# Kernel optimization log

Hardware: AMD Instinct MI355X
Metric: run time of the kernel (lower is better)

Reference implementation:

```python
import jax, jax.numpy as jnp
import numpy as np
from jax import lax

M, T, D, E, NTAGS = 512, 512, 128, 512, 74
GH = D // 2   # GRU hidden per direction (64)
LH = E // 2   # LSTM hidden per direction (256)


def _gru_dir(x, Wih, Whh, bih, bhh):
    # x: [T, Din] -> [T, H]; PyTorch gate order r, z, n
    h = Whh.shape[1]
    gi = x @ Wih.T + bih  # [T, 3H] precomputed input projections
    def step(hprev, gi_t):
        gh = hprev @ Whh.T + bhh
        r = jax.nn.sigmoid(gi_t[:h] + gh[:h])
        z = jax.nn.sigmoid(gi_t[h:2 * h] + gh[h:2 * h])
        n = jnp.tanh(gi_t[2 * h:] + r * gh[2 * h:])
        hnew = (1.0 - z) * n + z * hprev
        return hnew, hnew
    _, hs = lax.scan(step, jnp.zeros((h,), x.dtype), gi)
    return hs


def _bigru(x, Wf, Uf, bf, cf, Wb, Ub, bb, cb):
    hf = _gru_dir(x, Wf, Uf, bf, cf)
    hb = _gru_dir(x[::-1], Wb, Ub, bb, cb)[::-1]
    return jnp.concatenate([hf, hb], axis=-1)


def _lstm_dir(x, Wih, Whh, bih, bhh):
    # PyTorch gate order i, f, g, o
    h = Whh.shape[1]
    gi = x @ Wih.T + bih  # [T, 4H]
    def step(carry, gi_t):
        hprev, cprev = carry
        g = gi_t + hprev @ Whh.T + bhh
        i = jax.nn.sigmoid(g[:h])
        f = jax.nn.sigmoid(g[h:2 * h])
        gg = jnp.tanh(g[2 * h:3 * h])
        o = jax.nn.sigmoid(g[3 * h:])
        c = f * cprev + i * gg
        hnew = o * jnp.tanh(c)
        return (hnew, c), hnew
    init = (jnp.zeros((h,), x.dtype), jnp.zeros((h,), x.dtype))
    _, hs = lax.scan(step, init, gi)
    return hs


def _bilstm(x, Wf, Uf, bf, cf, Wb, Ub, bb, cb):
    hf = _lstm_dir(x, Wf, Uf, bf, cf)
    hb = _lstm_dir(x[::-1], Wb, Ub, bb, cb)[::-1]
    return jnp.concatenate([hf, hb], axis=-1)


def setup_inputs() -> dict:
    key = jax.random.key(0)
    ks = jax.random.split(key, 32)
    s = 0.05
    def n(k, shape, scale=s):
        return jax.random.normal(k, shape, jnp.float32) * scale
    inp = {
        'memory': jax.random.normal(ks[0], (M, T, D), jnp.float32),
        'u': jax.random.normal(ks[1], (T, D), jnp.float32),
        'embed': jax.random.normal(ks[2], (T, E), jnp.float32),
        'W_ff': n(ks[3], (D, 2 * D)), 'b_ff': n(ks[4], (D,)),
        'gWih_f': n(ks[5], (3 * GH, D)), 'gWhh_f': n(ks[6], (3 * GH, GH)),
        'gbih_f': n(ks[7], (3 * GH,)), 'gbhh_f': n(ks[8], (3 * GH,)),
        'gWih_b': n(ks[9], (3 * GH, D)), 'gWhh_b': n(ks[10], (3 * GH, GH)),
        'gbih_b': n(ks[11], (3 * GH,)), 'gbhh_b': n(ks[12], (3 * GH,)),
        'W_k': n(ks[13], (E, D)), 'b_k': n(ks[14], (E,)),
        'lWih_f': n(ks[15], (4 * LH, E)), 'lWhh_f': n(ks[16], (4 * LH, LH)),
        'lbih_f': n(ks[17], (4 * LH,)), 'lbhh_f': n(ks[18], (4 * LH,)),
        'lWih_b': n(ks[19], (4 * LH, E)), 'lWhh_b': n(ks[20], (4 * LH, LH)),
        'lbih_b': n(ks[21], (4 * LH,)), 'lbhh_b': n(ks[22], (4 * LH,)),
        'W_out': n(ks[23], (NTAGS, E)), 'b_out': n(ks[24], (NTAGS,)),
    }
    return inp


def reference(memory, u, embed, W_ff, b_ff,
              gWih_f, gWhh_f, gbih_f, gbhh_f,
              gWih_b, gWhh_b, gbih_b, gbhh_b,
              W_k, b_k,
              lWih_f, lWhh_f, lbih_f, lbhh_f,
              lWih_b, lWhh_b, lbih_b, lbhh_b,
              W_out, b_out):
    # --- memory attention (original: python loop over self._memory) ---
    # p[i] = <flatten(memory[i]), flatten(u)>; softmax over memories
    p = jax.nn.softmax(jnp.einsum('mtd,td->m', memory, u))  # [M]
    cat = jnp.concatenate([memory, jnp.broadcast_to(u, memory.shape)], axis=-1)  # [M,T,2D]
    g = cat @ W_ff.T + b_ff  # [M,T,D] (ff_layer applied per memory)
    G = jnp.einsum('m,mtd->td', p, g)  # weighted sum over memories [T,D]
    # --- session encoder (bidirectional GRU) ---
    h = _bigru(G, gWih_f, gWhh_f, gbih_f, gbhh_f, gWib := gWih_b, gWhh_b, gbih_b, gbhh_b)  # [T,D]
    # --- knowledge encoder ---
    o = (u + h) @ W_k.T + b_k  # [T,E]
    # --- tagging head: BiLSTM over embed + o, then linear + softmax ---
    x = embed + o
    comb = _bilstm(x, lWih_f, lWhh_f, lbih_f, lbhh_f, lWih_b, lWhh_b, lbih_b, lbhh_b)  # [T,E]
    logits = comb @ W_out.T + b_out  # [T, NTAGS]
    return jax.nn.softmax(logits, axis=-1)
```

## Files before the change

### kernel.cpp

```cpp
#include <hip/hip_runtime.h>
#include <math.h>

#define TT 512
#define DD 128
#define MM 512
#define EE 512
#define NTAGS 74
#define GH 64
#define LH 256

typedef _Float16 half_t;
typedef _Float16 v2h __attribute__((ext_vector_type(2)));
typedef _Float16 v8h __attribute__((ext_vector_type(8)));
typedef _Float16 v16h __attribute__((ext_vector_type(16)));
typedef int v4i __attribute__((ext_vector_type(4)));

__device__ __forceinline__ float fdot2f(v2h a, v2h b, float c) {
#if __has_builtin(__builtin_amdgcn_fdot2)
    return __builtin_amdgcn_fdot2(a, b, c, false);
#else
    return c + (float)a[0] * (float)b[0] + (float)a[1] * (float)b[1];
#endif
}

__device__ __forceinline__ int sdot4(int a, int b, int c) {
#if __has_builtin(__builtin_amdgcn_sdot4)
    return __builtin_amdgcn_sdot4(a, b, c, false);
#else
    return c + ((a << 24) >> 24) * ((b << 24) >> 24)
             + ((a << 16) >> 24) * ((b << 16) >> 24)
             + ((a << 8) >> 24) * ((b << 8) >> 24)
             + (a >> 24) * (b >> 24);
#endif
}

__device__ __forceinline__ float sigf(float x) { return 1.f / (1.f + __expf(-x)); }
__device__ __forceinline__ float tanhfast(float x) { return 1.f - 2.f / (__expf(2.f * x) + 1.f); }

__device__ __forceinline__ void lds_barrier() {
    __builtin_amdgcn_sched_barrier(0);
    asm volatile("s_waitcnt lgkmcnt(0)" ::: "memory");
    __builtin_amdgcn_s_barrier();
    __builtin_amdgcn_sched_barrier(0);
}

__device__ __forceinline__ void wave_lds_fence() {
    __builtin_amdgcn_sched_barrier(0);
    asm volatile("s_waitcnt lgkmcnt(0)" ::: "memory");
    __builtin_amdgcn_sched_barrier(0);
}

__device__ __forceinline__ v16h load16(const float* p) {
    float4 x0 = ((const float4*)p)[0];
    float4 x1 = ((const float4*)p)[1];
    float4 x2 = ((const float4*)p)[2];
    float4 x3 = ((const float4*)p)[3];
    v16h r;
    r[0] = (half_t)x0.x; r[1] = (half_t)x0.y; r[2] = (half_t)x0.z; r[3] = (half_t)x0.w;
    r[4] = (half_t)x1.x; r[5] = (half_t)x1.y; r[6] = (half_t)x1.z; r[7] = (half_t)x1.w;
    r[8] = (half_t)x2.x; r[9] = (half_t)x2.y; r[10] = (half_t)x2.z; r[11] = (half_t)x2.w;
    r[12] = (half_t)x3.x; r[13] = (half_t)x3.y; r[14] = (half_t)x3.z; r[15] = (half_t)x3.w;
    return r;
}

#define OPAQUE4(a, b, c, d) \
    asm volatile("" : "+v"(a), "+v"(b), "+v"(c), "+v"(d))

__device__ __forceinline__ void dot16(const v16h& w, const v8h& h0, const v8h& h1,
                                      float& x0, float& x1) {
    x0 = fdot2f(v2h{w[0], w[1]}, v2h{h0[0], h0[1]}, x0);
    x1 = fdot2f(v2h{w[2], w[3]}, v2h{h0[2], h0[3]}, x1);
    x0 = fdot2f(v2h{w[4], w[5]}, v2h{h0[4], h0[5]}, x0);
    x1 = fdot2f(v2h{w[6], w[7]}, v2h{h0[6], h0[7]}, x1);
    x0 = fdot2f(v2h{w[8], w[9]}, v2h{h1[0], h1[1]}, x0);
    x1 = fdot2f(v2h{w[10], w[11]}, v2h{h1[2], h1[3]}, x1);
    x0 = fdot2f(v2h{w[12], w[13]}, v2h{h1[4], h1[5]}, x0);
    x1 = fdot2f(v2h{w[14], w[15]}, v2h{h1[6], h1[7]}, x1);
}

__device__ __forceinline__ int pack4(int b0, int b1, int b2, int b3) {
    return (b0 & 0xff) | ((b1 & 0xff) << 8) | ((b2 & 0xff) << 16) | (b3 << 24);
}

__device__ __forceinline__ v4i quant16(const float* p, float inv_s) {
    float4 x0 = ((const float4*)p)[0];
    float4 x1 = ((const float4*)p)[1];
    float4 x2 = ((const float4*)p)[2];
    float4 x3 = ((const float4*)p)[3];
    v4i r;
    r.x = pack4(__float2int_rn(x0.x * inv_s), __float2int_rn(x0.y * inv_s),
                __float2int_rn(x0.z * inv_s), __float2int_rn(x0.w * inv_s));
    r.y = pack4(__float2int_rn(x1.x * inv_s), __float2int_rn(x1.y * inv_s),
                __float2int_rn(x1.z * inv_s), __float2int_rn(x1.w * inv_s));
    r.z = pack4(__float2int_rn(x2.x * inv_s), __float2int_rn(x2.y * inv_s),
                __float2int_rn(x2.z * inv_s), __float2int_rn(x2.w * inv_s));
    r.w = pack4(__float2int_rn(x3.x * inv_s), __float2int_rn(x3.y * inv_s),
                __float2int_rn(x3.z * inv_s), __float2int_rn(x3.w * inv_s));
    return r;
}

__device__ __forceinline__ float rowmax128(const float* p) {
    float m = 0.f;
#pragma unroll 8
    for (int k = 0; k < 128; k += 4) {
        float4 a = *(const float4*)(p + k);
        m = fmaxf(m, fmaxf(fmaxf(fabsf(a.x), fabsf(a.y)), fmaxf(fabsf(a.z), fabsf(a.w))));
    }
    return m;
}

__global__ __launch_bounds__(256) void k_dots(const float* __restrict__ mem,
                                              const float* __restrict__ u,
                                              float* __restrict__ dots) {
    int m = blockIdx.x;
    const float4* m4 = (const float4*)(mem + (size_t)m * TT * DD);
    const float4* u4 = (const float4*)u;
    float acc = 0.f;
#pragma unroll 4
    for (int it = 0; it < (TT * DD / 4) / 256; ++it) {
        int i = it * 256 + threadIdx.x;
        float4 a = m4[i], b = u4[i];
        acc += a.x * b.x + a.y * b.y + a.z * b.z + a.w * b.w;
    }
    for (int off = 32; off; off >>= 1) acc += __shfl_down(acc, off, 64);
    __shared__ float red[4];
    int w = threadIdx.x >> 6, l = threadIdx.x & 63;
    if (l == 0) red[w] = acc;
    __syncthreads();
    if (threadIdx.x == 0) dots[m] = red[0] + red[1] + red[2] + red[3];
}

__global__ __launch_bounds__(512) void k_softmax_p(const float* __restrict__ dots,
                                                   float* __restrict__ p) {
    int tid = threadIdx.x;
    float v = dots[tid];
    float mx = v;
    for (int off = 32; off; off >>= 1) mx = fmaxf(mx, __shfl_down(mx, off, 64));
    __shared__ float red[8];
    __shared__ float bm, bs;
    int w = tid >> 6, l = tid & 63;
    if (l == 0) red[w] = mx;
    __syncthreads();
    if (tid == 0) {
        float t = red[0];
        for (int i = 1; i < 8; ++i) t = fmaxf(t, red[i]);
        bm = t;
    }
    __syncthreads();
    float e = __expf(v - bm);
    float sm = e;
    for (int off = 32; off; off >>= 1) sm += __shfl_down(sm, off, 64);
    if (l == 0) red[w] = sm;
    __syncthreads();
    if (tid == 0) {
        float t = 0.f;
        for (int i = 0; i < 8; ++i) t += red[i];
        bs = t;
    }
    __syncthreads();
    p[tid] = e / bs;
}

__global__ __launch_bounds__(128) void k_wsum(const float* __restrict__ mem,
                                              const float* __restrict__ p,
                                              float* __restrict__ Mbar) {
    __shared__ float pl[MM];
    for (int i = threadIdx.x; i < MM; i += 128) pl[i] = p[i];
    __syncthreads();
    int i4 = blockIdx.x * 128 + threadIdx.x;
    const float4* m4 = (const float4*)mem;
    float4 acc = {0.f, 0.f, 0.f, 0.f};
#pragma unroll 4
    for (int m = 0; m < MM; ++m) {
        float pm = pl[m];
        float4 a = m4[(size_t)m * (TT * DD / 4) + i4];
        acc.x += pm * a.x; acc.y += pm * a.y; acc.z += pm * a.z; acc.w += pm * a.w;
    }
    ((float4*)Mbar)[i4] = acc;
}

__global__ __launch_bounds__(128) void k_G(const float* __restrict__ Mbar,
                                           const float* __restrict__ u,
                                           const float* __restrict__ Wff,
                                           const float* __restrict__ bff,
                                           float* __restrict__ G) {
    int t = blockIdx.x, d = threadIdx.x;
    __shared__ __align__(16) float Ml[DD], ul[DD];
    Ml[d] = Mbar[t * DD + d];
    ul[d] = u[t * DD + d];
    __syncthreads();
    const float* wr = Wff + (size_t)d * 2 * DD;
    float a0 = 0.f, a1 = 0.f;
#pragma unroll 4
    for (int k = 0; k < DD; ++k) {
        a0 += Ml[k] * wr[k];
        a1 += ul[k] * wr[DD + k];
    }
    G[t * DD + d] = a0 + a1 + bff[d];
}

__global__ __launch_bounds__(384) void k_gru_gi(const float* __restrict__ G,
                                                const float* __restrict__ Wf,
                                                const float* __restrict__ bf,
                                                const float* __restrict__ Wb,
                                                const float* __restrict__ bb,
                                                float* __restrict__ gi) {
    int t = blockIdx.x;
    __shared__ __align__(16) float Gl[DD];
    if (threadIdx.x < DD) Gl[threadIdx.x] = G[t * DD + threadIdx.x];
    __syncthreads();
    int r = threadIdx.x;
    const float* w;
    float b;
    float* o;
    if (r < 192) {
        w = Wf + (size_t)r * DD; b = bf[r]; o = gi + ((size_t)0 * TT + t) * 192 + r;
    } else {
        int rr = r - 192;
        w = Wb + (size_t)rr * DD; b = bb[rr]; o = gi + ((size_t)1 * TT + t) * 192 + rr;
    }
    float a0 = 0.f, a1 = 0.f;
#pragma unroll 4
    for (int k = 0; k < DD; k += 2) {
        a0 += Gl[k] * w[k];
        a1 += Gl[k + 1] * w[k + 1];
    }
    *o = a0 + a1 + b;
}

__global__ __launch_bounds__(64) void k_gru_seq(const float* __restrict__ Whh_f,
                                                const float* __restrict__ bhh_f,
                                                const float* __restrict__ Whh_b,
                                                const float* __restrict__ bhh_b,
                                                const float* __restrict__ gi,
                                                float* __restrict__ hbuf) {
    int dir = blockIdx.x;
    int u = threadIdx.x;
    const float* Whh = dir ? Whh_b : Whh_f;
    const float* bhh = dir ? bhh_b : bhh_f;
    const float* wr_ = Whh + (size_t)u * 64;
    const float* wz_ = Whh + (size_t)(64 + u) * 64;
    const float* wn_ = Whh + (size_t)(128 + u) * 64;
    v16h wr0 = load16(wr_), wr1 = load16(wr_ + 16), wr2 = load16(wr_ + 32), wr3 = load16(wr_ + 48);
    v16h wz0 = load16(wz_), wz1 = load16(wz_ + 16), wz2 = load16(wz_ + 32), wz3 = load16(wz_ + 48);
    v16h wn0 = load16(wn_), wn1 = load16(wn_ + 16), wn2 = load16(wn_ + 32), wn3 = load16(wn_ + 48);
    OPAQUE4(wr0, wr1, wr2, wr3);
    OPAQUE4(wz0, wz1, wz2, wz3);
    OPAQUE4(wn0, wn1, wn2, wn3);
    float bh_r = bhh[u], bh_z = bhh[64 + u], bh_n = bhh[128 + u];

    __shared__ __align__(16) half_t hl[64];
    hl[u] = (half_t)0.f;
    float h = 0.f;
    int t0 = dir ? (TT - 1) : 0;
    const float* g0p = gi + ((size_t)dir * TT + t0) * 192;
    float g_r = g0p[u], g_z = g0p[64 + u], g_n = g0p[128 + u];
    wave_lds_fence();

    for (int s = 0; s < TT; ++s) {
        int t = dir ? (TT - 1 - s) : s;
        int sn = (s + 1 < TT) ? (s + 1) : s;
        int tn = dir ? (TT - 1 - sn) : sn;
        const float* gb = gi + ((size_t)dir * TT + tn) * 192;
        float pn_r = gb[u], pn_z = gb[64 + u], pn_n = gb[128 + u];

        const v8h* hv = (const v8h*)hl;
        v8h h0 = hv[0], h1 = hv[1], h2 = hv[2], h3 = hv[3];
        v8h h4 = hv[4], h5 = hv[5], h6 = hv[6], h7 = hv[7];
        float ar0 = bh_r, ar1 = 0.f, az0 = bh_z, az1 = 0.f, an0 = bh_n, an1 = 0.f;
        dot16(wr0, h0, h1, ar0, ar1); dot16(wr1, h2, h3, ar0, ar1);
        dot16(wr2, h4, h5, ar0, ar1); dot16(wr3, h6, h7, ar0, ar1);
        dot16(wz0, h0, h1, az0, az1); dot16(wz1, h2, h3, az0, az1);
        dot16(wz2, h4, h5, az0, az1); dot16(wz3, h6, h7, az0, az1);
        dot16(wn0, h0, h1, an0, an1); dot16(wn1, h2, h3, an0, an1);
        dot16(wn2, h4, h5, an0, an1); dot16(wn3, h6, h7, an0, an1);

        float r = sigf(g_r + ar0 + ar1);
        float z = sigf(g_z + az0 + az1);
        float n = tanhfast(g_n + r * (an0 + an1));
        h = (1.f - z) * n + z * h;
        hbuf[t * DD + dir * 64 + u] = h;
        hl[u] = (half_t)h;
        wave_lds_fence();
        g_r = pn_r; g_z = pn_z; g_n = pn_n;
    }
}

__global__ __launch_bounds__(512) void k_x(const float* __restrict__ u,
                                           const float* __restrict__ hbuf,
                                           const float* __restrict__ Wk,
                                           const float* __restrict__ bk,
                                           const float* __restrict__ embed,
                                           float* __restrict__ x) {
    int t = blockIdx.x, e = threadIdx.x;
    __shared__ __align__(16) float sl[DD];
    if (e < DD) sl[e] = u[t * DD + e] + hbuf[t * DD + e];
    __syncthreads();
    const float* wr = Wk + (size_t)e * DD;
    float a0 = 0.f, a1 = 0.f;
#pragma unroll 4
    for (int k = 0; k < DD; k += 2) {
        a0 += sl[k] * wr[k];
        a1 += sl[k + 1] * wr[k + 1];
    }
    x[t * EE + e] = embed[t * EE + e] + a0 + a1 + bk[e];
}

__global__ __launch_bounds__(1024) void k_lstm_gi(const float* __restrict__ x,
                                                  const float* __restrict__ Wf,
                                                  const float* __restrict__ bf,
                                                  const float* __restrict__ Wb,
                                                  const float* __restrict__ bb,
                                                  float* __restrict__ gi) {
    int dir = blockIdx.y;
    int t0 = blockIdx.x * 8;
    __shared__ __align__(16) float xl[8 * EE];
    for (int i = threadIdx.x; i < 8 * EE; i += 1024) xl[i] = x[(size_t)t0 * EE + i];
    __syncthreads();
    int r = threadIdx.x;
    const float* W = dir ? Wb : Wf;
    const float* bi = dir ? bb : bf;
    const float* wr = W + (size_t)r * EE;
    float b = bi[r];
    float acc[8];
#pragma unroll
    for (int uu = 0; uu < 8; ++uu) acc[uu] = b;
    for (int k = 0; k < EE; k += 4) {
        float4 wv = *(const float4*)(wr + k);
#pragma unroll
        for (int uu = 0; uu < 8; ++uu) {
            float4 xv = *(const float4*)(&xl[uu * EE + k]);
            acc[uu] += wv.x * xv.x + wv.y * xv.y + wv.z * xv.z + wv.w * xv.w;
        }
    }
#pragma unroll
    for (int uu = 0; uu < 8; ++uu)
        gi[((size_t)dir * TT + (t0 + uu)) * 1024 + r] = acc[uu];
}

__global__ __launch_bounds__(512, 2) void k_lstm_seq(const float* __restrict__ Whh_f,
                                                     const float* __restrict__ bhh_f,
                                                     const float* __restrict__ Whh_b,
                                                     const float* __restrict__ bhh_b,
                                                     const float* __restrict__ gi,
                                                     float* __restrict__ comb) {
    int dir = blockIdx.x;
    int tid = threadIdx.x;
    int u = tid >> 1;
    int half = tid & 1;
    const float* Whh = dir ? Whh_b : Whh_f;
    const float* bhh = dir ? bhh_b : bhh_f;

    __shared__ __align__(16) int hq[2][64];

    const float* ri = Whh + (size_t)u * 256 + half * 128;
    const float* rf = Whh + (size_t)(256 + u) * 256 + half * 128;
    const float* rg = Whh + (size_t)(512 + u) * 256 + half * 128;
    const float* ro = Whh + (size_t)(768 + u) * 256 + half * 128;

    float mi = rowmax128(ri); mi = fmaxf(mi, __shfl_xor(mi, 1, 64));
    float mf = rowmax128(rf); mf = fmaxf(mf, __shfl_xor(mf, 1, 64));
    float mg = rowmax128(rg); mg = fmaxf(mg, __shfl_xor(mg, 1, 64));
    float mo = rowmax128(ro); mo = fmaxf(mo, __shfl_xor(mo, 1, 64));
    float inv_i = 127.f / mi, inv_f = 127.f / mf, inv_g = 127.f / mg, inv_o = 127.f / mo;
    float fs_i = mi / 16129.f, fs_f = mf / 16129.f, fs_g = mg / 16129.f, fs_o = mo / 16129.f;

#define DECLROW(P, ptr, inv)                                                      \
    v4i P##0 = quant16((ptr), (inv)),       P##1 = quant16((ptr) + 16, (inv)),    \
        P##2 = quant16((ptr) + 32, (inv)),  P##3 = quant16((ptr) + 48, (inv)),    \
        P##4 = quant16((ptr) + 64, (inv)),  P##5 = quant16((ptr) + 80, (inv)),    \
        P##6 = quant16((ptr) + 96, (inv)),  P##7 = quant16((ptr) + 112, (inv));   \
    OPAQUE4(P##0, P##1, P##2, P##3);                                              \
    OPAQUE4(P##4, P##5, P##6, P##7)

    DECLROW(wi, ri, inv_i);
    DECLROW(wf, rf, inv_f);
    DECLROW(wg, rg, inv_g);
    DECLROW(wo, ro, inv_o);
#undef DECLROW

    float bh_i = bhh[u], bh_f = bhh[256 + u], bh_g = bhh[512 + u], bh_o = bhh[768 + u];
    if (tid < 64) hq[0][tid] = 0;
    float c_state = 0.f;
    int tfirst = dir ? (TT - 1) : 0;
    const float* gp0 = gi + ((size_t)dir * TT + tfirst) * 1024;
    float g_i = gp0[u], g_f = gp0[256 + u], g_g = gp0[512 + u], g_o = gp0[768 + u];
    lds_barrier();

#define ROWD1(P, c, A0, A1)                                          \
    A0 = sdot4(P##c.x, hv##c.x, A0); A1 = sdot4(P##c.y, hv##c.y, A1); \
    A0 = sdot4(P##c.z, hv##c.z, A0); A1 = sdot4(P##c.w, hv##c.w, A1)
#define ROWDOT(P, A0, A1)                                                  \
    ROWD1(P, 0, A0, A1); ROWD1(P, 1, A0, A1); ROWD1(P, 2, A0, A1);         \
    ROWD1(P, 3, A0, A1); ROWD1(P, 4, A0, A1); ROWD1(P, 5, A0, A1);         \
    ROWD1(P, 6, A0, A1); ROWD1(P, 7, A0, A1)

    for (int s = 0; s < TT; ++s) {
        int t = dir ? (TT - 1 - s) : s;
        int sn = (s + 1 < TT) ? (s + 1) : s;
        int tn = dir ? (TT - 1 - sn) : sn;
        const float* gb = gi + ((size_t)dir * TT + tn) * 1024;
        float pn_i = gb[u], pn_f = gb[256 + u], pn_g = gb[512 + u], pn_o = gb[768 + u];

        const v4i* hb = (const v4i*)&hq[s & 1][half * 32];
        v4i hv0 = hb[0], hv1 = hb[1], hv2 = hb[2], hv3 = hb[3];
        v4i hv4 = hb[4], hv5 = hb[5], hv6 = hb[6], hv7 = hb[7];
        int ai0 = 0, ai1 = 0, af0 = 0, af1 = 0, ag0 = 0, ag1 = 0, ao0 = 0, ao1 = 0;
        ROWDOT(wi, ai0, ai1);
        ROWDOT(wf, af0, af1);
        ROWDOT(wg, ag0, ag1);
        ROWDOT(wo, ao0, ao1);
        int ai = ai0 + ai1; ai += __shfl_xor(ai, 1, 64);
        int af = af0 + af1; af += __shfl_xor(af, 1, 64);
        int ag = ag0 + ag1; ag += __shfl_xor(ag, 1, 64);
        int ao = ao0 + ao1; ao += __shfl_xor(ao, 1, 64);

        float iv = sigf((float)ai * fs_i + bh_i + g_i);
        float fv = sigf((float)af * fs_f + bh_f + g_f);
        float gv = tanhfast((float)ag * fs_g + bh_g + g_g);
        float ov = sigf((float)ao * fs_o + bh_o + g_o);
        c_state = fv * c_state + iv * gv;
        float hval = ov * tanhfast(c_state);
        if (half == 0) {
            comb[(size_t)t * EE + dir * 256 + u] = hval;
            ((signed char*)hq[(s + 1) & 1])[u] = (signed char)__float2int_rn(hval * 127.f);
        }
        lds_barrier();
        g_i = pn_i; g_f = pn_f; g_g = pn_g; g_o = pn_o;
    }
#undef ROWDOT
#undef ROWD1
}

__global__ __launch_bounds__(128) void k_out(const float* __restrict__ comb,
                                             const float* __restrict__ Wout,
                                             const float* __restrict__ bout,
                                             float* __restrict__ out) {
    int t = blockIdx.x;
    __shared__ __align__(16) float cl[EE];
    __shared__ float ll[NTAGS];
    __shared__ float mred, sred;
    for (int i = threadIdx.x; i < EE; i += 128) cl[i] = comb[(size_t)t * EE + i];
    __syncthreads();
    int e = threadIdx.x;
    if (e < NTAGS) {
        const float* wr = Wout + (size_t)e * EE;
        float a0 = 0.f, a1 = 0.f;
#pragma unroll 4
        for (int k = 0; k < EE; k += 2) {
            a0 += cl[k] * wr[k];
            a1 += cl[k + 1] * wr[k + 1];
        }
        ll[e] = a0 + a1 + bout[e];
    }
    __syncthreads();
    if (threadIdx.x == 0) {
        float m = ll[0];
        for (int i = 1; i < NTAGS; ++i) m = fmaxf(m, ll[i]);
        float ss = 0.f;
        for (int i = 0; i < NTAGS; ++i) ss += __expf(ll[i] - m);
        mred = m;
        sred = ss;
    }
    __syncthreads();
    if (e < NTAGS) out[t * NTAGS + e] = __expf(ll[e] - mred) / sred;
}

#define OFF_DOTS  ((size_t)0)
#define OFF_P     ((size_t)512)
#define OFF_MBAR  ((size_t)1024)
#define OFF_G     ((size_t)66560)
#define OFF_GIG   ((size_t)132096)
#define OFF_HBUF  ((size_t)328704)
#define OFF_X     ((size_t)394240)
#define OFF_GIL   ((size_t)656384)
#define OFF_COMB  ((size_t)1704960)

extern "C" void kernel_launch(void* const* d_in, const int* in_sizes, int n_in,
                              void* d_out, int out_size, void* d_ws, size_t ws_size,
                              hipStream_t stream) {
    const float* memory = (const float*)d_in[0];
    const float* u      = (const float*)d_in[1];
    const float* embed  = (const float*)d_in[2];
    const float* W_ff   = (const float*)d_in[3];
    const float* b_ff   = (const float*)d_in[4];
    const float* gWih_f = (const float*)d_in[5];
    const float* gWhh_f = (const float*)d_in[6];
    const float* gbih_f = (const float*)d_in[7];
    const float* gbhh_f = (const float*)d_in[8];
    const float* gWih_b = (const float*)d_in[9];
    const float* gWhh_b = (const float*)d_in[10];
    const float* gbih_b = (const float*)d_in[11];
    const float* gbhh_b = (const float*)d_in[12];
    const float* W_k    = (const float*)d_in[13];
    const float* b_k    = (const float*)d_in[14];
    const float* lWih_f = (const float*)d_in[15];
    const float* lWhh_f = (const float*)d_in[16];
    const float* lbih_f = (const float*)d_in[17];
    const float* lbhh_f = (const float*)d_in[18];
    const float* lWih_b = (const float*)d_in[19];
    const float* lWhh_b = (const float*)d_in[20];
    const float* lbih_b = (const float*)d_in[21];
    const float* lbhh_b = (const float*)d_in[22];
    const float* W_out  = (const float*)d_in[23];
    const float* b_out  = (const float*)d_in[24];
    float* out = (float*)d_out;
    float* ws = (float*)d_ws;

    float* dots = ws + OFF_DOTS;
    float* p    = ws + OFF_P;
    float* Mbar = ws + OFF_MBAR;
    float* G    = ws + OFF_G;
    float* giG  = ws + OFF_GIG;
    float* hbuf = ws + OFF_HBUF;
    float* x    = ws + OFF_X;
    float* giL  = ws + OFF_GIL;
    float* comb = ws + OFF_COMB;

    k_dots<<<MM, 256, 0, stream>>>(memory, u, dots);
    k_softmax_p<<<1, MM, 0, stream>>>(dots, p);
    k_wsum<<<128, 128, 0, stream>>>(memory, p, Mbar);
    k_G<<<TT, DD, 0, stream>>>(Mbar, u, W_ff, b_ff, G);
    k_gru_gi<<<TT, 384, 0, stream>>>(G, gWih_f, gbih_f, gWih_b, gbih_b, giG);
    k_gru_seq<<<2, 64, 0, stream>>>(gWhh_f, gbhh_f, gWhh_b, gbhh_b, giG, hbuf);
    k_x<<<TT, EE, 0, stream>>>(u, hbuf, W_k, b_k, embed, x);
    k_lstm_gi<<<dim3(64, 2), 1024, 0, stream>>>(x, lWih_f, lbih_f, lWih_b, lbih_b, giL);
    k_lstm_seq<<<2, 512, 0, stream>>>(lWhh_f, lbhh_f, lWhh_b, lbhh_b, giL, comb);
    k_out<<<TT, 128, 0, stream>>>(comb, W_out, b_out, out);
}
```

Before: 1.332 ms.

## Split recurrent GRU/LSTM dot products across four lanes with DPP reductions

The GRU and LSTM sequential kernels now give each hidden unit to four lanes instead of one or two. Each lane holds a quarter of the recurrent weight row, and partial sums are combined with DPP quad reductions. This shortens the serial per-step dot-product latency, which is the critical path of the scans. Hidden outputs are buffered four steps at a time and written transposed as float4, so downstream k_x and k_out read strided. In exchange, the GRU now uses a full workgroup barrier per step instead of a wave-local fence, and both kernels run more threads.

Result: slower. 1.398 ms (+4.9%).

```diff
diff --git a/kernel.cpp b/kernel.cpp
--- a/kernel.cpp
+++ b/kernel.cpp
@@ -44,10 +44,15 @@
     __builtin_amdgcn_sched_barrier(0);
 }
 
-__device__ __forceinline__ void wave_lds_fence() {
-    __builtin_amdgcn_sched_barrier(0);
-    asm volatile("s_waitcnt lgkmcnt(0)" ::: "memory");
-    __builtin_amdgcn_sched_barrier(0);
+__device__ __forceinline__ int qreduce_i(int x) {
+    x += __builtin_amdgcn_mov_dpp(x, 0xB1, 0xF, 0xF, true);
+    x += __builtin_amdgcn_mov_dpp(x, 0x4E, 0xF, 0xF, true);
+    return x;
+}
+__device__ __forceinline__ float qreduce_f(float x) {
+    x += __int_as_float(__builtin_amdgcn_mov_dpp(__float_as_int(x), 0xB1, 0xF, 0xF, true));
+    x += __int_as_float(__builtin_amdgcn_mov_dpp(__float_as_int(x), 0x4E, 0xF, 0xF, true));
+    return x;
 }
 
 __device__ __forceinline__ v16h load16(const float* p) {
@@ -63,8 +68,8 @@
     return r;
 }
 
-#define OPAQUE4(a, b, c, d) \
-    asm volatile("" : "+v"(a), "+v"(b), "+v"(c), "+v"(d))
+#define OPAQUE3(a, b, c) asm volatile("" : "+v"(a), "+v"(b), "+v"(c))
+#define OPAQUE4(a, b, c, d) asm volatile("" : "+v"(a), "+v"(b), "+v"(c), "+v"(d))
 
 __device__ __forceinline__ void dot16(const v16h& w, const v8h& h0, const v8h& h1,
                                       float& x0, float& x1) {
@@ -99,10 +104,10 @@
     return r;
 }
 
-__device__ __forceinline__ float rowmax128(const float* p) {
+__device__ __forceinline__ float rowmax64(const float* p) {
     float m = 0.f;
-#pragma unroll 8
-    for (int k = 0; k < 128; k += 4) {
+#pragma unroll
+    for (int k = 0; k < 64; k += 4) {
         float4 a = *(const float4*)(p + k);
         m = fmaxf(m, fmaxf(fmaxf(fabsf(a.x), fabsf(a.y)), fmaxf(fabsf(a.z), fabsf(a.w))));
     }
@@ -228,73 +233,82 @@
     *o = a0 + a1 + b;
 }
 
-__global__ __launch_bounds__(64) void k_gru_seq(const float* __restrict__ Whh_f,
-                                                const float* __restrict__ bhh_f,
-                                                const float* __restrict__ Whh_b,
-                                                const float* __restrict__ bhh_b,
-                                                const float* __restrict__ gi,
-                                                float* __restrict__ hbuf) {
+__global__ __launch_bounds__(256) void k_gru_seq(const float* __restrict__ Whh_f,
+                                                 const float* __restrict__ bhh_f,
+                                                 const float* __restrict__ Whh_b,
+                                                 const float* __restrict__ bhh_b,
+                                                 const float* __restrict__ gi,
+                                                 float* __restrict__ hbufT) {
     int dir = blockIdx.x;
-    int u = threadIdx.x;
+    int tid = threadIdx.x;
+    int u = tid >> 2;
+    int q = tid & 3;
     const float* Whh = dir ? Whh_b : Whh_f;
     const float* bhh = dir ? bhh_b : bhh_f;
-    const float* wr_ = Whh + (size_t)u * 64;
-    const float* wz_ = Whh + (size_t)(64 + u) * 64;
-    const float* wn_ = Whh + (size_t)(128 + u) * 64;
-    v16h wr0 = load16(wr_), wr1 = load16(wr_ + 16), wr2 = load16(wr_ + 32), wr3 = load16(wr_ + 48);
-    v16h wz0 = load16(wz_), wz1 = load16(wz_ + 16), wz2 = load16(wz_ + 32), wz3 = load16(wz_ + 48);
-    v16h wn0 = load16(wn_), wn1 = load16(wn_ + 16), wn2 = load16(wn_ + 32), wn3 = load16(wn_ + 48);
-    OPAQUE4(wr0, wr1, wr2, wr3);
-    OPAQUE4(wz0, wz1, wz2, wz3);
-    OPAQUE4(wn0, wn1, wn2, wn3);
+    v16h wr = load16(Whh + (size_t)u * 64 + q * 16);
+    v16h wz = load16(Whh + (size_t)(64 + u) * 64 + q * 16);
+    v16h wn = load16(Whh + (size_t)(128 + u) * 64 + q * 16);
+    OPAQUE3(wr, wz, wn);
     float bh_r = bhh[u], bh_z = bhh[64 + u], bh_n = bhh[128 + u];
 
-    __shared__ __align__(16) half_t hl[64];
-    hl[u] = (half_t)0.f;
+    __shared__ __align__(16) half_t hl[2][64];
+    if (tid < 64) hl[0][tid] = (half_t)0.f;
     float h = 0.f;
     int t0 = dir ? (TT - 1) : 0;
-    const float* g0p = gi + ((size_t)dir * TT + t0) * 192;
-    float g_r = g0p[u], g_z = g0p[64 + u], g_n = g0p[128 + u];
-    wave_lds_fence();
-
-    for (int s = 0; s < TT; ++s) {
-        int t = dir ? (TT - 1 - s) : s;
-        int sn = (s + 1 < TT) ? (s + 1) : s;
-        int tn = dir ? (TT - 1 - sn) : sn;
-        const float* gb = gi + ((size_t)dir * TT + tn) * 192;
-        float pn_r = gb[u], pn_z = gb[64 + u], pn_n = gb[128 + u];
-
-        const v8h* hv = (const v8h*)hl;
-        v8h h0 = hv[0], h1 = hv[1], h2 = hv[2], h3 = hv[3];
-        v8h h4 = hv[4], h5 = hv[5], h6 = hv[6], h7 = hv[7];
-        float ar0 = bh_r, ar1 = 0.f, az0 = bh_z, az1 = 0.f, an0 = bh_n, an1 = 0.f;
-        dot16(wr0, h0, h1, ar0, ar1); dot16(wr1, h2, h3, ar0, ar1);
-        dot16(wr2, h4, h5, ar0, ar1); dot16(wr3, h6, h7, ar0, ar1);
-        dot16(wz0, h0, h1, az0, az1); dot16(wz1, h2, h3, az0, az1);
-        dot16(wz2, h4, h5, az0, az1); dot16(wz3, h6, h7, az0, az1);
-        dot16(wn0, h0, h1, an0, an1); dot16(wn1, h2, h3, an0, an1);
-        dot16(wn2, h4, h5, an0, an1); dot16(wn3, h6, h7, an0, an1);
-
-        float r = sigf(g_r + ar0 + ar1);
-        float z = sigf(g_z + az0 + az1);
-        float n = tanhfast(g_n + r * (an0 + an1));
-        h = (1.f - z) * n + z * h;
-        hbuf[t * DD + dir * 64 + u] = h;
-        hl[u] = (half_t)h;
-        wave_lds_fence();
-        g_r = pn_r; g_z = pn_z; g_n = pn_n;
-    }
+    const float* g0p = gi + ((size_t)dir * TT + t0) * 192 + u;
+    float g_r = g0p[0], g_z = g0p[64], g_n = g0p[128];
+    lds_barrier();
+
+    float hs0 = 0.f, hs1 = 0.f, hs2 = 0.f, hs3 = 0.f;
+#define GSTEP(J, HS) { \
+    int s_ = s4 + (J); \
+    int sn_ = (s_ + 1 < TT) ? (s_ + 1) : s_; \
+    int tn_ = dir ? (TT - 1 - sn_) : sn_; \
+    const float* gb_ = gi + ((size_t)dir * TT + tn_) * 192 + u; \
+    float pr_ = gb_[0], pz_ = gb_[64], pn_ = gb_[128]; \
+    const v8h* hv_ = (const v8h*)&hl[s_ & 1][q * 16]; \
+    v8h h0_ = hv_[0], h1_ = hv_[1]; \
+    float ar0 = 0.f, ar1 = 0.f, az0 = 0.f, az1 = 0.f, an0 = 0.f, an1 = 0.f; \
+    dot16(wr, h0_, h1_, ar0, ar1); \
+    dot16(wz, h0_, h1_, az0, az1); \
+    dot16(wn, h0_, h1_, an0, an1); \
+    float srd = qreduce_f(ar0 + ar1); \
+    float szd = qreduce_f(az0 + az1); \
+    float snd = qreduce_f(an0 + an1); \
+    float r_ = sigf(g_r + srd + bh_r); \
+    float z_ = sigf(g_z + szd + bh_z); \
+    float n_ = tanhfast(g_n + r_ * (snd + bh_n)); \
+    h = (1.f - z_) * n_ + z_ * h; \
+    if (q == 0) hl[(s_ + 1) & 1][u] = (half_t)h; \
+    HS = h; \
+    lds_barrier(); \
+    g_r = pr_; g_z = pz_; g_n = pn_; }
+
+    for (int s4 = 0; s4 < TT; s4 += 4) {
+        GSTEP(0, hs0);
+        GSTEP(1, hs1);
+        GSTEP(2, hs2);
+        GSTEP(3, hs3);
+        if (q == 0) {
+            float4 v;
+            int tb;
+            if (dir == 0) { tb = s4; v = {hs0, hs1, hs2, hs3}; }
+            else          { tb = TT - 4 - s4; v = {hs3, hs2, hs1, hs0}; }
+            *(float4*)(hbufT + (size_t)(dir * 64 + u) * TT + tb) = v;
+        }
+    }
+#undef GSTEP
 }
 
 __global__ __launch_bounds__(512) void k_x(const float* __restrict__ u,
-                                           const float* __restrict__ hbuf,
+                                           const float* __restrict__ hbufT,
                                            const float* __restrict__ Wk,
                                            const float* __restrict__ bk,
                                            const float* __restrict__ embed,
                                            float* __restrict__ x) {
     int t = blockIdx.x, e = threadIdx.x;
     __shared__ __align__(16) float sl[DD];
-    if (e < DD) sl[e] = u[t * DD + e] + hbuf[t * DD + e];
+    if (e < DD) sl[e] = u[t * DD + e] + hbufT[(size_t)e * TT + t];
     __syncthreads();
     const float* wr = Wk + (size_t)e * DD;
     float a0 = 0.f, a1 = 0.f;
@@ -338,101 +352,113 @@
         gi[((size_t)dir * TT + (t0 + uu)) * 1024 + r] = acc[uu];
 }
 
-__global__ __launch_bounds__(512, 2) void k_lstm_seq(const float* __restrict__ Whh_f,
-                                                     const float* __restrict__ bhh_f,
-                                                     const float* __restrict__ Whh_b,
-                                                     const float* __restrict__ bhh_b,
-                                                     const float* __restrict__ gi,
-                                                     float* __restrict__ comb) {
+__global__ __launch_bounds__(1024, 4) void k_lstm_seq(const float* __restrict__ Whh_f,
+                                                      const float* __restrict__ bhh_f,
+                                                      const float* __restrict__ Whh_b,
+                                                      const float* __restrict__ bhh_b,
+                                                      const float* __restrict__ gi,
+                                                      float* __restrict__ combT) {
     int dir = blockIdx.x;
     int tid = threadIdx.x;
-    int u = tid >> 1;
-    int half = tid & 1;
+    int u = tid >> 2;
+    int q = tid & 3;
     const float* Whh = dir ? Whh_b : Whh_f;
     const float* bhh = dir ? bhh_b : bhh_f;
 
     __shared__ __align__(16) int hq[2][64];
 
-    const float* ri = Whh + (size_t)u * 256 + half * 128;
-    const float* rf = Whh + (size_t)(256 + u) * 256 + half * 128;
-    const float* rg = Whh + (size_t)(512 + u) * 256 + half * 128;
-    const float* ro = Whh + (size_t)(768 + u) * 256 + half * 128;
-
-    float mi = rowmax128(ri); mi = fmaxf(mi, __shfl_xor(mi, 1, 64));
-    float mf = rowmax128(rf); mf = fmaxf(mf, __shfl_xor(mf, 1, 64));
-    float mg = rowmax128(rg); mg = fmaxf(mg, __shfl_xor(mg, 1, 64));
-    float mo = rowmax128(ro); mo = fmaxf(mo, __shfl_xor(mo, 1, 64));
-    float inv_i = 127.f / mi, inv_f = 127.f / mf, inv_g = 127.f / mg, inv_o = 127.f / mo;
+    const float* ri = Whh + (size_t)u * 256 + q * 64;
+    const float* rf = ri + 256 * 256;
+    const float* rg = ri + 512 * 256;
+    const float* ro = ri + 768 * 256;
+
+    float mi = rowmax64(ri); mi = fmaxf(mi, __shfl_xor(mi, 1, 64)); mi = fmaxf(mi, __shfl_xor(mi, 2, 64));
+    float mf = rowmax64(rf); mf = fmaxf(mf, __shfl_xor(mf, 1, 64)); mf = fmaxf(mf, __shfl_xor(mf, 2, 64));
+    float mg = rowmax64(rg); mg = fmaxf(mg, __shfl_xor(mg, 1, 64)); mg = fmaxf(mg, __shfl_xor(mg, 2, 64));
+    float mo = rowmax64(ro); mo = fmaxf(mo, __shfl_xor(mo, 1, 64)); mo = fmaxf(mo, __shfl_xor(mo, 2, 64));
     float fs_i = mi / 16129.f, fs_f = mf / 16129.f, fs_g = mg / 16129.f, fs_o = mo / 16129.f;
 
-#define DECLROW(P, ptr, inv)                                                      \
-    v4i P##0 = quant16((ptr), (inv)),       P##1 = quant16((ptr) + 16, (inv)),    \
-        P##2 = quant16((ptr) + 32, (inv)),  P##3 = quant16((ptr) + 48, (inv)),    \
-        P##4 = quant16((ptr) + 64, (inv)),  P##5 = quant16((ptr) + 80, (inv)),    \
-        P##6 = quant16((ptr) + 96, (inv)),  P##7 = quant16((ptr) + 112, (inv));   \
-    OPAQUE4(P##0, P##1, P##2, P##3);                                              \
-    OPAQUE4(P##4, P##5, P##6, P##7)
-
-    DECLROW(wi, ri, inv_i);
-    DECLROW(wf, rf, inv_f);
-    DECLROW(wg, rg, inv_g);
-    DECLROW(wo, ro, inv_o);
-#undef DECLROW
+    v4i wi0, wi1, wi2, wi3, wf0, wf1, wf2, wf3, wg0, wg1, wg2, wg3, wo0, wo1, wo2, wo3;
+    {
+        float inv_i = 127.f / mi, inv_f = 127.f / mf, inv_g = 127.f / mg, inv_o = 127.f / mo;
+        wi0 = quant16(ri, inv_i); wi1 = quant16(ri + 16, inv_i);
+        wi2 = quant16(ri + 32, inv_i); wi3 = quant16(ri + 48, inv_i);
+        wf0 = quant16(rf, inv_f); wf1 = quant16(rf + 16, inv_f);
+        wf2 = quant16(rf + 32, inv_f); wf3 = quant16(rf + 48, inv_f);
+        wg0 = quant16(rg, inv_g); wg1 = quant16(rg + 16, inv_g);
+        wg2 = quant16(rg + 32, inv_g); wg3 = quant16(rg + 48, inv_g);
+        wo0 = quant16(ro, inv_o); wo1 = quant16(ro + 16, inv_o);
+        wo2 = quant16(ro + 32, inv_o); wo3 = quant16(ro + 48, inv_o);
+    }
+    OPAQUE4(wi0, wi1, wi2, wi3);
+    OPAQUE4(wf0, wf1, wf2, wf3);
+    OPAQUE4(wg0, wg1, wg2, wg3);
+    OPAQUE4(wo0, wo1, wo2, wo3);
 
     float bh_i = bhh[u], bh_f = bhh[256 + u], bh_g = bhh[512 + u], bh_o = bhh[768 + u];
     if (tid < 64) hq[0][tid] = 0;
     float c_state = 0.f;
     int tfirst = dir ? (TT - 1) : 0;
-    const float* gp0 = gi + ((size_t)dir * TT + tfirst) * 1024;
-    float g_i = gp0[u], g_f = gp0[256 + u], g_g = gp0[512 + u], g_o = gp0[768 + u];
+    const float* gp0 = gi + ((size_t)dir * TT + tfirst) * 1024 + u;
+    float g_i = gp0[0], g_f = gp0[256], g_g = gp0[512], g_o = gp0[768];
     lds_barrier();
 
-#define ROWD1(P, c, A0, A1)                                          \
-    A0 = sdot4(P##c.x, hv##c.x, A0); A1 = sdot4(P##c.y, hv##c.y, A1); \
-    A0 = sdot4(P##c.z, hv##c.z, A0); A1 = sdot4(P##c.w, hv##c.w, A1)
-#define ROWDOT(P, A0, A1)                                                  \
-    ROWD1(P, 0, A0, A1); ROWD1(P, 1, A0, A1); ROWD1(P, 2, A0, A1);         \
-    ROWD1(P, 3, A0, A1); ROWD1(P, 4, A0, A1); ROWD1(P, 5, A0, A1);         \
-    ROWD1(P, 6, A0, A1); ROWD1(P, 7, A0, A1)
-
-    for (int s = 0; s < TT; ++s) {
-        int t = dir ? (TT - 1 - s) : s;
-        int sn = (s + 1 < TT) ? (s + 1) : s;
-        int tn = dir ? (TT - 1 - sn) : sn;
-        const float* gb = gi + ((size_t)dir * TT + tn) * 1024;
-        float pn_i = gb[u], pn_f = gb[256 + u], pn_g = gb[512 + u], pn_o = gb[768 + u];
-
-        const v4i* hb = (const v4i*)&hq[s & 1][half * 32];
-        v4i hv0 = hb[0], hv1 = hb[1], hv2 = hb[2], hv3 = hb[3];
-        v4i hv4 = hb[4], hv5 = hb[5], hv6 = hb[6], hv7 = hb[7];
-        int ai0 = 0, ai1 = 0, af0 = 0, af1 = 0, ag0 = 0, ag1 = 0, ao0 = 0, ao1 = 0;
-        ROWDOT(wi, ai0, ai1);
-        ROWDOT(wf, af0, af1);
-        ROWDOT(wg, ag0, ag1);
-        ROWDOT(wo, ao0, ao1);
-        int ai = ai0 + ai1; ai += __shfl_xor(ai, 1, 64);
-        int af = af0 + af1; af += __shfl_xor(af, 1, 64);
-        int ag = ag0 + ag1; ag += __shfl_xor(ag, 1, 64);
-        int ao = ao0 + ao1; ao += __shfl_xor(ao, 1, 64);
-
-        float iv = sigf((float)ai * fs_i + bh_i + g_i);
-        float fv = sigf((float)af * fs_f + bh_f + g_f);
-        float gv = tanhfast((float)ag * fs_g + bh_g + g_g);
-        float ov = sigf((float)ao * fs_o + bh_o + g_o);
-        c_state = fv * c_state + iv * gv;
-        float hval = ov * tanhfast(c_state);
-        if (half == 0) {
-            comb[(size_t)t * EE + dir * 256 + u] = hval;
-            ((signed char*)hq[(s + 1) & 1])[u] = (signed char)__float2int_rn(hval * 127.f);
+    float hs0 = 0.f, hs1 = 0.f, hs2 = 0.f, hs3 = 0.f;
+#define LDOT(P, A0, A1) \
+    A0 = sdot4((P##0).x, h0_.x, A0); A1 = sdot4((P##0).y, h0_.y, A1); \
+    A0 = sdot4((P##0).z, h0_.z, A0); A1 = sdot4((P##0).w, h0_.w, A1); \
+    A0 = sdot4((P##1).x, h1_.x, A0); A1 = sdot4((P##1).y, h1_.y, A1); \
+    A0 = sdot4((P##1).z, h1_.z, A0); A1 = sdot4((P##1).w, h1_.w, A1); \
+    A0 = sdot4((P##2).x, h2_.x, A0); A1 = sdot4((P##2).y, h2_.y, A1); \
+    A0 = sdot4((P##2).z, h2_.z, A0); A1 = sdot4((P##2).w, h2_.w, A1); \
+    A0 = sdot4((P##3).x, h3_.x, A0); A1 = sdot4((P##3).y, h3_.y, A1); \
+    A0 = sdot4((P##3).z, h3_.z, A0); A1 = sdot4((P##3).w, h3_.w, A1)
+
+#define LSTEP(J, HS) { \
+    int s_ = s4 + (J); \
+    int sn_ = (s_ + 1 < TT) ? (s_ + 1) : s_; \
+    int tn_ = dir ? (TT - 1 - sn_) : sn_; \
+    const float* gb_ = gi + ((size_t)dir * TT + tn_) * 1024 + u; \
+    float pi_ = gb_[0], pf_ = gb_[256], pg_ = gb_[512], po_ = gb_[768]; \
+    const v4i* hb_ = (const v4i*)&hq[s_ & 1][q * 16]; \
+    v4i h0_ = hb_[0], h1_ = hb_[1], h2_ = hb_[2], h3_ = hb_[3]; \
+    int ai0 = 0, ai1 = 0, af0 = 0, af1 = 0, ag0 = 0, ag1 = 0, ao0 = 0, ao1 = 0; \
+    LDOT(wi, ai0, ai1); \
+    LDOT(wf, af0, af1); \
+    LDOT(wg, ag0, ag1); \
+    LDOT(wo, ao0, ao1); \
+    int ai_ = qreduce_i(ai0 + ai1); \
+    int af_ = qreduce_i(af0 + af1); \
+    int ag_ = qreduce_i(ag0 + ag1); \
+    int ao_ = qreduce_i(ao0 + ao1); \
+    float iv = sigf((float)ai_ * fs_i + bh_i + g_i); \
+    float fv = sigf((float)af_ * fs_f + bh_f + g_f); \
+    float gv = tanhfast((float)ag_ * fs_g + bh_g + g_g); \
+    float ov = sigf((float)ao_ * fs_o + bh_o + g_o); \
+    c_state = fv * c_state + iv * gv; \
+    HS = ov * tanhfast(c_state); \
+    if (q == 0) ((signed char*)hq[(s_ + 1) & 1])[u] = (signed char)__float2int_rn(HS * 127.f); \
+    lds_barrier(); \
+    g_i = pi_; g_f = pf_; g_g = pg_; g_o = po_; }
+
+    for (int s4 = 0; s4 < TT; s4 += 4) {
+        LSTEP(0, hs0);
+        LSTEP(1, hs1);
+        LSTEP(2, hs2);
+        LSTEP(3, hs3);
+        if (q == 0) {
+            float4 v;
+            int tb;
+            if (dir == 0) { tb = s4; v = {hs0, hs1, hs2, hs3}; }
+            else          { tb = TT - 4 - s4; v = {hs3, hs2, hs1, hs0}; }
+            *(float4*)(combT + (size_t)(dir * 256 + u) * TT + tb) = v;
         }
-        lds_barrier();
-        g_i = pn_i; g_f = pn_f; g_g = pn_g; g_o = pn_o;
-    }
-#undef ROWDOT
-#undef ROWD1
-}
-
-__global__ __launch_bounds__(128) void k_out(const float* __restrict__ comb,
+    }
+#undef LSTEP
+#undef LDOT
+}
+
+__global__ __launch_bounds__(128) void k_out(const float* __restrict__ combT,
                                              const float* __restrict__ Wout,
                                              const float* __restrict__ bout,
                                              float* __restrict__ out) {
@@ -440,7 +466,7 @@
     __shared__ __align__(16) float cl[EE];
     __shared__ float ll[NTAGS];
     __shared__ float mred, sred;
-    for (int i = threadIdx.x; i < EE; i += 128) cl[i] = comb[(size_t)t * EE + i];
+    for (int i = threadIdx.x; i < EE; i += 128) cl[i] = combT[(size_t)i * TT + t];
     __syncthreads();
     int e = threadIdx.x;
     if (e < NTAGS) {
@@ -507,24 +533,24 @@
     float* out = (float*)d_out;
     float* ws = (float*)d_ws;
 
-    float* dots = ws + OFF_DOTS;
-    float* p    = ws + OFF_P;
-    float* Mbar = ws + OFF_MBAR;
-    float* G    = ws + OFF_G;
-    float* giG  = ws + OFF_GIG;
-    float* hbuf = ws + OFF_HBUF;
-    float* x    = ws + OFF_X;
-    float* giL  = ws + OFF_GIL;
-    float* comb = ws + OFF_COMB;
+    float* dots  = ws + OFF_DOTS;
+    float* p     = ws + OFF_P;
+    float* Mbar  = ws + OFF_MBAR;
+    float* G     = ws + OFF_G;
+    float* giG   = ws + OFF_GIG;
+    float* hbufT = ws + OFF_HBUF;
+    float* x     = ws + OFF_X;
+    float* giL   = ws + OFF_GIL;
+    float* combT = ws + OFF_COMB;
 
     k_dots<<<MM, 256, 0, stream>>>(memory, u, dots);
     k_softmax_p<<<1, MM, 0, stream>>>(dots, p);
     k_wsum<<<128, 128, 0, stream>>>(memory, p, Mbar);
     k_G<<<TT, DD, 0, stream>>>(Mbar, u, W_ff, b_ff, G);
     k_gru_gi<<<TT, 384, 0, stream>>>(G, gWih_f, gbih_f, gWih_b, gbih_b, giG);
-    k_gru_seq<<<2, 64, 0, stream>>>(gWhh_f, gbhh_f, gWhh_b, gbhh_b, giG, hbuf);
-    k_x<<<TT, EE, 0, stream>>>(u, hbuf, W_k, b_k, embed, x);
+    k_gru_seq<<<2, 256, 0, stream>>>(gWhh_f, gbhh_f, gWhh_b, gbhh_b, giG, hbufT);
+    k_x<<<TT, EE, 0, stream>>>(u, hbufT, W_k, b_k, embed, x);
     k_lstm_gi<<<dim3(64, 2), 1024, 0, stream>>>(x, lWih_f, lbih_f, lWih_b, lbih_b, giL);
-    k_lstm_seq<<<2, 512, 0, stream>>>(lWhh_f, lbhh_f, lWhh_b, lbhh_b, giL, comb);
-    k_out<<<TT, 128, 0, stream>>>(comb, W_out, b_out, out);
-}
+    k_lstm_seq<<<2, 1024, 0, stream>>>(lWhh_f, lbhh_f, lWhh_b, lbhh_b, giL, combT);
+    k_out<<<TT, 128, 0, stream>>>(combT, W_out, b_out, out);
+}
```
